# Performance work log

Hardware: AMD Instinct MI355X
Metric: run time of the kernel (lower is better)

## Reference

```python
import jax, jax.numpy as jnp
import numpy as np

H, HKV, DH, T_MAX = 32, 8, 128, 4096
ROPE_BASE = 500000.0


def apply_rope(x, pos, base):
    # x: [B, h, T, D]; MLX rope, traditional=False (split-half rotation)
    B, h, T, D = x.shape
    half = D // 2
    inv_freq = 1.0 / (base ** (jnp.arange(half, dtype=jnp.float32) * 2.0 / D))
    t = (pos + jnp.arange(T)).astype(jnp.float32)  # absolute positions
    ang = t[:, None] * inv_freq[None, :]           # [T, half]
    cos = jnp.cos(ang)[None, None]                 # [1,1,T,half]
    sin = jnp.sin(ang)[None, None]
    x1, x2 = x[..., :half], x[..., half:]
    return jnp.concatenate([x1 * cos - x2 * sin, x2 * cos + x1 * sin], axis=-1)


def setup_inputs() -> dict:
    key = jax.random.key(0)
    ks = jax.random.split(key, 5)
    hidden = 4096
    return {
        "hidden_states": jax.random.normal(ks[0], (1, 2048, hidden), jnp.float32),
        "Wq": jax.random.normal(ks[1], (hidden, H * DH), jnp.float32) * 0.02,
        "Wk": jax.random.normal(ks[2], (hidden, HKV * DH), jnp.float32) * 0.02,
        "Wv": jax.random.normal(ks[3], (hidden, HKV * DH), jnp.float32) * 0.02,
        "Wo": jax.random.normal(ks[4], (H * DH, hidden), jnp.float32) * 0.02,
        "pos_int": 0,
    }


def reference(hidden_states, Wq, Wk, Wv, Wo, pos_int):
    B, T, _ = hidden_states.shape
    q = (hidden_states @ Wq).reshape(B, T, H, DH).transpose(0, 2, 1, 3)    # [B,H,T,D]
    k = (hidden_states @ Wk).reshape(B, T, HKV, DH).transpose(0, 2, 1, 3)  # [B,Hkv,T,D]
    v = (hidden_states @ Wv).reshape(B, T, HKV, DH).transpose(0, 2, 1, 3)

    q = apply_rope(q, pos_int, ROPE_BASE)
    k = apply_rope(k, pos_int, ROPE_BASE)

    # KV cache: write at [pos:pos+T], then slice [:pos+T] (pos is static Python int)
    k_cache = jnp.zeros((B, HKV, T_MAX, DH), jnp.float32)
    v_cache = jnp.zeros((B, HKV, T_MAX, DH), jnp.float32)
    k_cache = jax.lax.dynamic_update_slice(k_cache, k, (0, 0, pos_int, 0))
    v_cache = jax.lax.dynamic_update_slice(v_cache, v, (0, 0, pos_int, 0))
    end_pos = pos_int + T
    k_ = k_cache[:, :, :end_pos, :]  # [B,Hkv,S,D]
    v_ = v_cache[:, :, :end_pos, :]
    S = end_pos

    # GQA without materializing repeat_interleave: group query heads per kv head
    group = H // HKV
    qg = q.reshape(B, HKV, group, T, DH)
    scale = 1.0 / jnp.sqrt(jnp.float32(DH))
    scores = jnp.einsum("bhgtd,bhsd->bhgts", qg, k_) * scale  # [B,Hkv,g,T,S]
    # torch SDPA is_causal=True: top-left aligned mask (allow s <= t)
    causal = jnp.arange(S)[None, :] <= jnp.arange(T)[:, None]  # [T,S]
    scores = jnp.where(causal[None, None, None], scores, -jnp.inf)
    probs = jax.nn.softmax(scores, axis=-1)
    attn = jnp.einsum("bhgts,bhsd->bhgtd", probs, v_)          # [B,Hkv,g,T,D]
    attn = attn.reshape(B, H, T, DH).transpose(0, 2, 1, 3).reshape(B, T, H * DH)
    return attn @ Wo
```

## Files before the change

kernel.cpp:

```cpp
#include <hip/hip_runtime.h>
#include <hip/hip_bf16.h>
#include <math.h>

typedef unsigned short u16;
typedef __attribute__((ext_vector_type(4))) float f32x4;
typedef __attribute__((ext_vector_type(8))) short bf16x8;

#define GLD16(gptr, lptr) __builtin_amdgcn_global_load_lds( \
    (const __attribute__((address_space(1))) void*)(gptr),  \
    (__attribute__((address_space(3))) void*)(lptr), 16, 0, 0)

__device__ __forceinline__ float bf2f(u16 u) {
  union { unsigned int i; float f; } c; c.i = ((unsigned int)u) << 16; return c.f;
}
__device__ __forceinline__ u16 f2bf(float f) {
  union { float f; unsigned int i; } c; c.f = f;
  unsigned int r = c.i + 0x7fffu + ((c.i >> 16) & 1u);
  return (u16)(r >> 16);
}

__global__ __launch_bounds__(256) void f32_to_bf16(const float* __restrict__ in,
                                                   u16* __restrict__ out, int n4) {
  int i = blockIdx.x * 256 + threadIdx.x;
  if (i >= n4) return;
  float4 v = reinterpret_cast<const float4*>(in)[i];
  ushort4 o;
  o.x = f2bf(v.x); o.y = f2bf(v.y); o.z = f2bf(v.z); o.w = f2bf(v.w);
  reinterpret_cast<ushort4*>(out)[i] = o;
}

__global__ __launch_bounds__(256) void transpose_convert(const float* __restrict__ W,
                                                         u16* __restrict__ Wt,
                                                         int K, int N) {
  __shared__ float tile[32][33];
  const int n0 = blockIdx.x * 32, k0 = blockIdx.y * 32;
  const int tx = threadIdx.x & 31, ty = threadIdx.x >> 5;
#pragma unroll
  for (int r = 0; r < 32; r += 8)
    tile[ty + r][tx] = W[(size_t)(k0 + ty + r) * N + (n0 + tx)];
  __syncthreads();
#pragma unroll
  for (int r = 0; r < 32; r += 8)
    Wt[(size_t)(n0 + ty + r) * K + (k0 + tx)] = f2bf(tile[tx][ty + r]);
}

__global__ __launch_bounds__(256) void transpose_v(const u16* __restrict__ Vsrc,
                                                   u16* __restrict__ Vt) {
  __shared__ u16 tile[32][33];
  const int t0 = blockIdx.x * 32, d0 = blockIdx.y * 32, hkv = blockIdx.z;
  const int tx = threadIdx.x & 31, ty = threadIdx.x >> 5;
#pragma unroll
  for (int r = 0; r < 32; r += 8)
    tile[ty + r][tx] = Vsrc[(size_t)(t0 + ty + r) * 6144 + hkv * 128 + d0 + tx];
  __syncthreads();
#pragma unroll
  for (int r = 0; r < 32; r += 8)
    Vt[((size_t)hkv * 128 + d0 + ty + r) * 2048 + t0 + tx] = tile[tx][ty + r];
}

__global__ __launch_bounds__(256) void rope_table(float2* __restrict__ tab,
                                                  const int* __restrict__ pos_ptr) {
  int idx = blockIdx.x * 256 + threadIdx.x;
  int d = idx & 63, t = idx >> 6;
  int pos = *pos_ptr;
  float inv = exp2f(-(float)d * (0.015625f * 18.931568569324174f));
  float ang = (float)(pos + t) * inv;
  tab[idx] = make_float2(cosf(ang), sinf(ang));
}

__global__ __launch_bounds__(256) void rope_apply(u16* __restrict__ X, int nheads,
                                                  int stride,
                                                  const float2* __restrict__ tab) {
  int idx = blockIdx.x * 256 + threadIdx.x;
  int total = 2048 * nheads * 64;
  if (idx >= total) return;
  int d = idx & 63;
  int h = (idx >> 6) % nheads;
  int t = idx / (64 * nheads);
  float2 cs = tab[t * 64 + d];
  size_t base = (size_t)t * stride + h * 128 + d;
  float x1 = bf2f(X[base]);
  float x2 = bf2f(X[base + 64]);
  X[base]      = f2bf(x1 * cs.x - x2 * cs.y);
  X[base + 64] = f2bf(x2 * cs.x + x1 * cs.y);
}

template <int OUT_BF16>
__global__ __launch_bounds__(256) void gemm_db(const u16* __restrict__ A,
                                               const u16* __restrict__ Bt,
                                               void* __restrict__ C,
                                               int M, int N, int K) {
  __shared__ alignas(16) u16 As[2][128 * 64];
  __shared__ alignas(16) u16 Bs[2][128 * 64];
  const int tid = threadIdx.x;
  const int w = tid >> 6, lane = tid & 63;
  const int l15 = lane & 15, lg = lane >> 4;
  const int wr = w >> 1, wc = w & 1;
  const int m0 = blockIdx.y * 128, n0 = blockIdx.x * 128;
  const int wvb = tid & ~63;

  f32x4 acc[4][4];
#pragma unroll
  for (int i = 0; i < 4; ++i)
#pragma unroll
    for (int j = 0; j < 4; ++j) {
      f32x4 z = {0.f, 0.f, 0.f, 0.f};
      acc[i][j] = z;
    }

#define STAGE(s_, b_)                                                           \
  do {                                                                          \
    _Pragma("unroll")                                                           \
    for (int p = 0; p < 4; ++p) {                                               \
      const int slot = p * 256 + tid;                                           \
      const int row = slot >> 3, ch = slot & 7;                                 \
      const int col = (ch ^ (row & 7)) * 8;                                     \
      GLD16(A + (size_t)(m0 + row) * K + (s_) * 64 + col,                       \
            &As[b_][(p * 256 + wvb) * 8]);                                      \
      GLD16(Bt + (size_t)(n0 + row) * K + (s_) * 64 + col,                      \
            &Bs[b_][(p * 256 + wvb) * 8]);                                      \
    }                                                                           \
  } while (0)

  STAGE(0, 0);
  __syncthreads();
  int cur = 0;

  const int nt = K >> 6;
  for (int t = 0; t < nt; ++t) {
    if (t + 1 < nt) STAGE(t + 1, cur ^ 1);
#pragma unroll
    for (int ks = 0; ks < 2; ++ks) {
      bf16x8 af[4], bfr[4];
#pragma unroll
      for (int i = 0; i < 4; ++i) {
        const int row = wr * 64 + i * 16 + l15;
        const int ch = (ks * 4 + lg) ^ (row & 7);
        af[i] = *reinterpret_cast<const bf16x8*>(&As[cur][row * 64 + ch * 8]);
      }
#pragma unroll
      for (int j = 0; j < 4; ++j) {
        const int row = wc * 64 + j * 16 + l15;
        const int ch = (ks * 4 + lg) ^ (row & 7);
        bfr[j] = *reinterpret_cast<const bf16x8*>(&Bs[cur][row * 64 + ch * 8]);
      }
      __builtin_amdgcn_s_setprio(1);
#pragma unroll
      for (int i = 0; i < 4; ++i)
#pragma unroll
        for (int j = 0; j < 4; ++j)
          acc[i][j] = __builtin_amdgcn_mfma_f32_16x16x32_bf16(af[i], bfr[j], acc[i][j], 0, 0, 0);
      __builtin_amdgcn_s_setprio(0);
    }
    __syncthreads();
    cur ^= 1;
  }
#undef STAGE

#pragma unroll
  for (int i = 0; i < 4; ++i)
#pragma unroll
    for (int j = 0; j < 4; ++j)
#pragma unroll
      for (int r = 0; r < 4; ++r) {
        const int row = m0 + wr * 64 + i * 16 + lg * 4 + r;
        const int col = n0 + wc * 64 + j * 16 + l15;
        const float v = acc[i][j][r];
        if (OUT_BF16) ((u16*)C)[(size_t)row * N + col] = f2bf(v);
        else          ((float*)C)[(size_t)row * N + col] = v;
      }
}

__global__ __launch_bounds__(256) void attn_kernel(const u16* __restrict__ Q,
                                                   const u16* __restrict__ K,
                                                   const u16* __restrict__ Vt,
                                                   u16* __restrict__ O,
                                                   const int* __restrict__ pos_ptr) {
  const int pos = *pos_ptr;
  const int h = blockIdx.y;
  const int hkv = h >> 2;
  const int tid = threadIdx.x;
  const int w = tid >> 6, lane = tid & 63;
  const int l15 = lane & 15, lg = lane >> 4;

  __shared__ alignas(16) u16 Ks[2][64 * 128];
  __shared__ alignas(16) u16 Vs[2][128 * 64];
  __shared__ alignas(16) u16 Pl[4][16][72];

  const u16* Kh = K + hkv * 128;
  const u16* Vh = Vt + (size_t)hkv * 128 * 2048;

  const float C = 0.12752961957823275f;
  const float THR = 62.0f;
  const int wvb = tid & ~63;

#define STAGE_TILE(st_, b_)                                                        \
  do {                                                                             \
    const int s0_ = (st_) * 64;                                                    \
    _Pragma("unroll")                                                              \
    for (int p = 0; p < 4; ++p) {                                                  \
      const int idx = p * 256 + tid;                                               \
      const int kr = idx >> 4, kc = (idx & 15) ^ (kr & 7);                         \
      GLD16(Kh + (size_t)(s0_ + kr) * 6144 + kc * 8, &Ks[b_][(p * 256 + wvb) * 8]);\
      const int vr = idx >> 3, vc = (idx & 7) ^ (vr & 7);                          \
      GLD16(Vh + (size_t)vr * 2048 + s0_ + vc * 8, &Vs[b_][(p * 256 + wvb) * 8]);  \
    }                                                                              \
  } while (0)

  for (int pass = 0; pass < 2; ++pass) {
    const int qb = (pass == 0) ? (8 + (int)blockIdx.x) : (7 - (int)blockIdx.x);
    const int qt0 = qb * 128;
    const int nst = 2 * qb + 2;

    bf16x8 qa[2][4];
#pragma unroll
    for (int f = 0; f < 2; ++f) {
      const int qrow = qt0 + w * 32 + f * 16 + l15;
#pragma unroll
      for (int kk = 0; kk < 4; ++kk)
        qa[f][kk] = *reinterpret_cast<const bf16x8*>(
            Q + (size_t)qrow * 6144 + h * 128 + kk * 32 + lg * 8);
    }

    f32x4 acc[2][8];
#pragma unroll
    for (int f = 0; f < 2; ++f)
#pragma unroll
      for (int i = 0; i < 8; ++i) { f32x4 z = {0.f, 0.f, 0.f, 0.f}; acc[f][i] = z; }
    float mrun[2][4], lpart[2][4];
#pragma unroll
    for (int f = 0; f < 2; ++f)
#pragma unroll
      for (int r = 0; r < 4; ++r) {
        mrun[f][r] = (pos > 0) ? 0.0f : -INFINITY;
        lpart[f][r] = 0.0f;
      }

    STAGE_TILE(0, 0);
    __syncthreads();
    int cur = 0;

    for (int st = 0; st < nst; ++st) {
      if (st + 1 < nst) STAGE_TILE(st + 1, cur ^ 1);
      const int s0 = st * 64;

#pragma unroll
      for (int f = 0; f < 2; ++f) {
        const int frag_base = qt0 + w * 32 + f * 16;

        float pv[4][4];
        __builtin_amdgcn_s_setprio(1);
#pragma unroll
        for (int sub = 0; sub < 4; ++sub) {
          f32x4 s4 = {0.f, 0.f, 0.f, 0.f};
          const int row = sub * 16 + l15;
#pragma unroll
          for (int kk = 0; kk < 4; ++kk) {
            const int chunk = (kk * 4 + lg) ^ (row & 7);
            bf16x8 kf = *reinterpret_cast<const bf16x8*>(&Ks[cur][row * 128 + chunk * 8]);
            s4 = __builtin_amdgcn_mfma_f32_16x16x32_bf16(qa[f][kk], kf, s4, 0, 0, 0);
          }
#pragma unroll
          for (int r = 0; r < 4; ++r) pv[sub][r] = s4[r];
        }
        __builtin_amdgcn_s_setprio(0);

        if (s0 + 64 > frag_base) {
#pragma unroll
          for (int r = 0; r < 4; ++r) {
            const int qrow = frag_base + lg * 4 + r;
#pragma unroll
            for (int sub = 0; sub < 4; ++sub) {
              const int scol = s0 + sub * 16 + l15;
              pv[sub][r] = (scol <= qrow) ? pv[sub][r] : -INFINITY;
            }
          }
        }

        float lmax[4];
#pragma unroll
        for (int r = 0; r < 4; ++r)
          lmax[r] = fmaxf(fmaxf(pv[0][r], pv[1][r]), fmaxf(pv[2][r], pv[3][r]));
        float dml = fmaxf(fmaxf(lmax[0] - mrun[f][0], lmax[1] - mrun[f][1]),
                          fmaxf(lmax[2] - mrun[f][2], lmax[3] - mrun[f][3]));
        if (!__all(dml <= THR)) {
          float sfr[4];
#pragma unroll
          for (int r = 0; r < 4; ++r) {
            float mx = lmax[r];
#pragma unroll
            for (int off = 1; off < 16; off <<= 1) mx = fmaxf(mx, __shfl_xor(mx, off));
            const float mnew = fmaxf(mrun[f][r], mx);
            sfr[r] = exp2f((mrun[f][r] - mnew) * C);
            mrun[f][r] = mnew;
            lpart[f][r] *= sfr[r];
          }
#pragma unroll
          for (int dc = 0; dc < 8; ++dc)
#pragma unroll
            for (int r = 0; r < 4; ++r) acc[f][dc][r] *= sfr[r];
        }

#pragma unroll
        for (int r = 0; r < 4; ++r) {
          const float nmC = -mrun[f][r] * C;
          float ps = 0.0f;
#pragma unroll
          for (int sub = 0; sub < 4; ++sub) {
            const float p = exp2f(fmaf(pv[sub][r], C, nmC));
            pv[sub][r] = p;
            ps += p;
          }
          lpart[f][r] += ps;
        }

#pragma unroll
        for (int sub = 0; sub < 4; ++sub)
#pragma unroll
          for (int r = 0; r < 4; ++r)
            Pl[w][lg * 4 + r][sub * 16 + l15] = f2bf(pv[sub][r]);

        __builtin_amdgcn_s_setprio(1);
#pragma unroll
        for (int ks = 0; ks < 2; ++ks) {
          bf16x8 pf = *reinterpret_cast<const bf16x8*>(&Pl[w][l15][ks * 32 + lg * 8]);
#pragma unroll
          for (int dc = 0; dc < 8; ++dc) {
            const int row = dc * 16 + l15;
            const int chunk = (ks * 4 + lg) ^ (row & 7);
            bf16x8 vf = *reinterpret_cast<const bf16x8*>(&Vs[cur][row * 64 + chunk * 8]);
            acc[f][dc] = __builtin_amdgcn_mfma_f32_16x16x32_bf16(pf, vf, acc[f][dc], 0, 0, 0);
          }
        }
        __builtin_amdgcn_s_setprio(0);
      }

      __syncthreads();
      cur ^= 1;
    }

#pragma unroll
    for (int f = 0; f < 2; ++f)
#pragma unroll
      for (int r = 0; r < 4; ++r) {
        float l = lpart[f][r];
#pragma unroll
        for (int off = 1; off < 16; off <<= 1) l += __shfl_xor(l, off);
        if (pos > 0) l += (float)pos * exp2f(-mrun[f][r] * C);
        const float linv = 1.0f / l;
        const int qrow = qt0 + w * 32 + f * 16 + lg * 4 + r;
#pragma unroll
        for (int dc = 0; dc < 8; ++dc)
          O[(size_t)qrow * 4096 + h * 128 + dc * 16 + l15] = f2bf(acc[f][dc][r] * linv);
      }
  }
#undef STAGE_TILE
}

extern "C" void kernel_launch(void* const* d_in, const int* in_sizes, int n_in,
                              void* d_out, int out_size, void* d_ws, size_t ws_size,
                              hipStream_t stream) {
  const float* hs = (const float*)d_in[0];
  const float* Wq = (const float*)d_in[1];
  const float* Wk = (const float*)d_in[2];
  const float* Wv = (const float*)d_in[3];
  const float* Wo = (const float*)d_in[4];
  const int* pos  = (const int*)d_in[5];

  char* ws = (char*)d_ws;
  u16* hs_bf = (u16*)(ws + 0);
  u16* WT    = (u16*)(ws + 16777216ULL);
  u16* QKVb  = (u16*)(ws + 67108864ULL);
  u16* attnO = hs_bf;
  u16* WoT   = WT;
  u16* Vtg   = (u16*)(ws + 50331648ULL);
  float2* tabF = (float2*)(ws + 54525952ULL);

  f32_to_bf16<<<8192, 256, 0, stream>>>(hs, hs_bf, 2097152);
  transpose_convert<<<dim3(128, 128), 256, 0, stream>>>(Wq, WT, 4096, 4096);
  transpose_convert<<<dim3(32, 128), 256, 0, stream>>>(Wk, WT + (size_t)4096 * 4096, 4096, 1024);
  transpose_convert<<<dim3(32, 128), 256, 0, stream>>>(Wv, WT + (size_t)5120 * 4096, 4096, 1024);

  gemm_db<1><<<dim3(48, 16), 256, 0, stream>>>(hs_bf, WT, QKVb, 2048, 6144, 4096);

  transpose_convert<<<dim3(128, 128), 256, 0, stream>>>(Wo, WoT, 4096, 4096);

  rope_table<<<512, 256, 0, stream>>>(tabF, pos);
  rope_apply<<<16384, 256, 0, stream>>>(QKVb, 32, 6144, tabF);
  rope_apply<<<4096, 256, 0, stream>>>(QKVb + 4096, 8, 6144, tabF);

  transpose_v<<<dim3(64, 4, 8), 256, 0, stream>>>(QKVb + 5120, Vtg);

  attn_kernel<<<dim3(8, 32), 256, 0, stream>>>(QKVb, QKVb + 4096, Vtg, attnO, pos);

  gemm_db<0><<<dim3(32, 16), 256, 0, stream>>>(attnO, WoT, d_out, 2048, 4096, 4096);
}
```

Before: 395.6 us.

## Enlarge GEMM tiles to 256x256 with 512-thread blocks and swizzled block order

```diff
diff --git a/kernel.cpp b/kernel.cpp
--- a/kernel.cpp
+++ b/kernel.cpp
@@ -86,22 +86,27 @@
 }
 
 template <int OUT_BF16>
-__global__ __launch_bounds__(256) void gemm_db(const u16* __restrict__ A,
-                                               const u16* __restrict__ Bt,
-                                               void* __restrict__ C,
-                                               int M, int N, int K) {
-  __shared__ alignas(16) u16 As[2][128 * 64];
-  __shared__ alignas(16) u16 Bs[2][128 * 64];
+__global__ __launch_bounds__(512, 2) void gemm_big(const u16* __restrict__ A,
+                                                   const u16* __restrict__ Bt,
+                                                   void* __restrict__ C,
+                                                   int M, int N, int K) {
+  __shared__ alignas(16) u16 As[2][256 * 64];
+  __shared__ alignas(16) u16 Bs[2][256 * 64];
   const int tid = threadIdx.x;
-  const int w = tid >> 6, lane = tid & 63;
+  const int lane = tid & 63, wid = tid >> 6;
   const int l15 = lane & 15, lg = lane >> 4;
-  const int wr = w >> 1, wc = w & 1;
-  const int m0 = blockIdx.y * 128, n0 = blockIdx.x * 128;
+  const int wm = wid >> 2, wn = wid & 3;
   const int wvb = tid & ~63;
 
-  f32x4 acc[4][4];
-#pragma unroll
-  for (int i = 0; i < 4; ++i)
+  const int nwg = gridDim.x * gridDim.y;
+  const int id0 = blockIdx.y * gridDim.x + blockIdx.x;
+  const int id = (id0 & 7) * (nwg >> 3) + (id0 >> 3);
+  const int n0 = (id % gridDim.x) * 256;
+  const int m0 = (id / gridDim.x) * 256;
+
+  f32x4 acc[8][4];
+#pragma unroll
+  for (int i = 0; i < 8; ++i)
 #pragma unroll
     for (int j = 0; j < 4; ++j) {
       f32x4 z = {0.f, 0.f, 0.f, 0.f};
@@ -112,13 +117,13 @@
   do {                                                                          \
     _Pragma("unroll")                                                           \
     for (int p = 0; p < 4; ++p) {                                               \
-      const int slot = p * 256 + tid;                                           \
+      const int slot = p * 512 + tid;                                           \
       const int row = slot >> 3, ch = slot & 7;                                 \
       const int col = (ch ^ (row & 7)) * 8;                                     \
       GLD16(A + (size_t)(m0 + row) * K + (s_) * 64 + col,                       \
-            &As[b_][(p * 256 + wvb) * 8]);                                      \
+            &As[b_][(p * 512 + wvb) * 8]);                                      \
       GLD16(Bt + (size_t)(n0 + row) * K + (s_) * 64 + col,                      \
-            &Bs[b_][(p * 256 + wvb) * 8]);                                      \
+            &Bs[b_][(p * 512 + wvb) * 8]);                                      \
     }                                                                           \
   } while (0)
 
@@ -130,23 +135,23 @@
   for (int t = 0; t < nt; ++t) {
     if (t + 1 < nt) STAGE(t + 1, cur ^ 1);
 #pragma unroll
-    for (int ks = 0; ks < 2; ++ks) {
-      bf16x8 af[4], bfr[4];
-#pragma unroll
-      for (int i = 0; i < 4; ++i) {
-        const int row = wr * 64 + i * 16 + l15;
-        const int ch = (ks * 4 + lg) ^ (row & 7);
+    for (int g = 0; g < 2; ++g) {
+      bf16x8 af[8], bfr[4];
+#pragma unroll
+      for (int i = 0; i < 8; ++i) {
+        const int row = wm * 128 + i * 16 + l15;
+        const int ch = (g * 4 + lg) ^ (row & 7);
         af[i] = *reinterpret_cast<const bf16x8*>(&As[cur][row * 64 + ch * 8]);
       }
 #pragma unroll
       for (int j = 0; j < 4; ++j) {
-        const int row = wc * 64 + j * 16 + l15;
-        const int ch = (ks * 4 + lg) ^ (row & 7);
+        const int row = wn * 64 + j * 16 + l15;
+        const int ch = (g * 4 + lg) ^ (row & 7);
         bfr[j] = *reinterpret_cast<const bf16x8*>(&Bs[cur][row * 64 + ch * 8]);
       }
       __builtin_amdgcn_s_setprio(1);
 #pragma unroll
-      for (int i = 0; i < 4; ++i)
+      for (int i = 0; i < 8; ++i)
 #pragma unroll
         for (int j = 0; j < 4; ++j)
           acc[i][j] = __builtin_amdgcn_mfma_f32_16x16x32_bf16(af[i], bfr[j], acc[i][j], 0, 0, 0);
@@ -158,13 +163,13 @@
 #undef STAGE
 
 #pragma unroll
-  for (int i = 0; i < 4; ++i)
+  for (int i = 0; i < 8; ++i)
 #pragma unroll
     for (int j = 0; j < 4; ++j)
 #pragma unroll
       for (int r = 0; r < 4; ++r) {
-        const int row = m0 + wr * 64 + i * 16 + lg * 4 + r;
-        const int col = n0 + wc * 64 + j * 16 + l15;
+        const int row = m0 + wm * 128 + i * 16 + lg * 4 + r;
+        const int col = n0 + wn * 64 + j * 16 + l15;
         const float v = acc[i][j][r];
         if (OUT_BF16) ((u16*)C)[(size_t)row * N + col] = f2bf(v);
         else          ((float*)C)[(size_t)row * N + col] = v;
@@ -381,7 +386,7 @@
   transpose_convert<<<dim3(32, 128), 256, 0, stream>>>(Wk, WT + (size_t)4096 * 4096, 4096, 1024);
   transpose_convert<<<dim3(32, 128), 256, 0, stream>>>(Wv, WT + (size_t)5120 * 4096, 4096, 1024);
 
-  gemm_db<1><<<dim3(48, 16), 256, 0, stream>>>(hs_bf, WT, QKVb, 2048, 6144, 4096);
+  gemm_big<1><<<dim3(24, 8), 512, 0, stream>>>(hs_bf, WT, QKVb, 2048, 6144, 4096);
 
   transpose_convert<<<dim3(128, 128), 256, 0, stream>>>(Wo, WoT, 4096, 4096);
 
@@ -393,5 +398,5 @@
 
   attn_kernel<<<dim3(8, 32), 256, 0, stream>>>(QKVb, QKVb + 4096, Vtg, attnO, pos);
 
-  gemm_db<0><<<dim3(32, 16), 256, 0, stream>>>(attnO, WoT, d_out, 2048, 4096, 4096);
-}
+  gemm_big<0><<<dim3(16, 8), 512, 0, stream>>>(attnO, WoT, d_out, 2048, 4096, 4096);
+}
```

Result: slower. 446.4 us (+12.8%).
